# Optimization experiments

Measured on AMD Instinct MI355X. Metric: run time of the kernel, lower is better.

Reference implementation:

```python
import jax, jax.numpy as jnp
import numpy as np

N_NODES = 50000
N_EDGES = 1600000
IN_CH = 128
HID = 128  # 2 * out_channels
NUM_GRAPHS = 64


def gcn_conv(x, row, col, ew, W, b, num_nodes):
    # PyG GCNConv: add self-loops (weight 1), symmetric degree norm, x @ W,
    # gather at source row, scale by norm, scatter-add at target col, add bias.
    loop = jnp.arange(num_nodes)
    r = jnp.concatenate([row, loop])
    c = jnp.concatenate([col, loop])
    w = jnp.concatenate([ew, jnp.ones((num_nodes,), ew.dtype)])
    deg = jax.ops.segment_sum(w, c, num_segments=num_nodes)
    dis = jnp.where(deg > 0, jax.lax.rsqrt(jnp.where(deg > 0, deg, 1.0)), 0.0)
    norm = dis[r] * w * dis[c]  # [E+N]
    xw = x @ W  # [N, HID]
    msg = xw[r] * norm[:, None]  # [E+N, HID] gather + scale
    out = jax.ops.segment_sum(msg, c, num_segments=num_nodes)
    return out + b


def setup_inputs() -> dict:
    key = jax.random.key(0)
    ks = jax.random.split(key, 8)
    x = jax.random.normal(ks[0], (N_NODES, IN_CH), dtype=jnp.float32)
    edge_index = jax.random.randint(ks[1], (2, N_EDGES), 0, N_NODES, dtype=jnp.int64)
    edge_weight = jax.random.uniform(ks[2], (N_EDGES,), dtype=jnp.float32)
    batch = jnp.sort(jax.random.randint(ks[3], (N_NODES,), 0, NUM_GRAPHS, dtype=jnp.int64))
    W1 = jax.random.normal(ks[4], (IN_CH, HID), dtype=jnp.float32) * 0.01
    b1 = jnp.zeros((HID,), jnp.float32)
    W2 = jax.random.normal(ks[5], (HID, HID), dtype=jnp.float32) * 0.01
    b2 = jnp.zeros((HID,), jnp.float32)
    return {"x": x, "edge_index": edge_index, "edge_weight": edge_weight,
            "batch": batch, "W1": W1, "b1": b1, "W2": W2, "b2": b2}


def reference(x, edge_index, edge_weight, batch, W1, b1, W2, b2):
    row, col = edge_index[0], edge_index[1]
    h = jax.nn.relu(gcn_conv(x, row, col, edge_weight, W1, b1, N_NODES))
    h = jax.nn.relu(gcn_conv(h, row, col, edge_weight, W2, b2, N_NODES))
    # global_mean_pool over batch segment ids
    sums = jax.ops.segment_sum(h, batch, num_segments=NUM_GRAPHS)
    cnts = jax.ops.segment_sum(jnp.ones((N_NODES,), h.dtype), batch, num_segments=NUM_GRAPHS)
    pooled = sums / jnp.maximum(cnts, 1.0)[:, None]
    return h, pooled
```

## Files before the change

### kernel.cpp

```cpp
#include <hip/hip_runtime.h>


#define CH 128
#define BSH 7
#define NBLK 1024
#define MAXNB 512
#define PCH 32
#define LDW 136

typedef __attribute__((ext_vector_type(8))) short bf16x8;
typedef __attribute__((ext_vector_type(4))) float f32x4;

static __device__ __forceinline__ unsigned short f2bf(float f) {
    unsigned u = __float_as_uint(f);
    unsigned r = (u + 0x7FFF + ((u >> 16) & 1)) >> 16;
    return (unsigned short)r;
}
static __device__ __forceinline__ float bflo(unsigned v) { return __uint_as_float(v << 16); }
static __device__ __forceinline__ float bfhi(unsigned v) { return __uint_as_float(v & 0xFFFF0000u); }

__global__ __launch_bounds__(256) void k_sort1a(const int* __restrict__ col,
                                                int* __restrict__ H, int E, int NB, int chunk) {
    __shared__ int hist[MAXNB];
    int t = threadIdx.x, blk = blockIdx.x;
    for (int i = t; i < NB; i += 256) hist[i] = 0;
    __syncthreads();
    int s = blk * chunk, e1 = min(s + chunk, E);
    for (int e = s + t; e < e1; e += 256) atomicAdd(&hist[col[e] >> BSH], 1);
    __syncthreads();
    for (int i = t; i < NB; i += 256) H[(size_t)i * NBLK + blk] = hist[i];
}

__global__ __launch_bounds__(1024) void k_scan1(int* __restrict__ data,
                                                int* __restrict__ bsum, int n) {
    __shared__ int sd[1024];
    int t = threadIdx.x;
    int i = blockIdx.x * 1024 + t;
    int v = (i < n) ? data[i] : 0;
    sd[t] = v;
    __syncthreads();
    for (int off = 1; off < 1024; off <<= 1) {
        int u = (t >= off) ? sd[t - off] : 0;
        __syncthreads();
        sd[t] += u;
        __syncthreads();
    }
    if (i < n) data[i] = sd[t] - v;
    if (t == 1023) bsum[blockIdx.x] = sd[1023];
}

__global__ __launch_bounds__(1024) void k_scan2(int* bsum, int nb, int* total) {
    __shared__ int sd[1024];
    int t = threadIdx.x;
    int v = (t < nb) ? bsum[t] : 0;
    sd[t] = v;
    __syncthreads();
    for (int off = 1; off < 1024; off <<= 1) {
        int u = (t >= off) ? sd[t - off] : 0;
        __syncthreads();
        sd[t] += u;
        __syncthreads();
    }
    if (t < nb) bsum[t] = sd[t] - v;
    if (t == 1023) *total = sd[1023];
}

__global__ __launch_bounds__(256) void k_sort1b(const int* __restrict__ row,
                                                const int* __restrict__ col,
                                                const float* __restrict__ ew,
                                                const int* __restrict__ Hs,
                                                const int* __restrict__ bsum,
                                                int2* __restrict__ pairs2,
                                                int E, int NB, int chunk) {
    __shared__ int cur[MAXNB];
    int t = threadIdx.x, blk = blockIdx.x;
    for (int i = t; i < NB; i += 256) cur[i] = Hs[(size_t)i * NBLK + blk] + bsum[i];
    __syncthreads();
    int s = blk * chunk, e1 = min(s + chunk, E);
    for (int e = s + t; e < e1; e += 256) {
        int c = col[e];
        int pos = atomicAdd(&cur[c >> BSH], 1);
        pairs2[pos] = make_int2(row[e] | ((c & 127) << 17), __float_as_int(ew[e]));
    }
}

__global__ __launch_bounds__(256) void k_sort2(const int* __restrict__ Hs,
                                               const int* __restrict__ bsum,
                                               const int2* __restrict__ pairs2,
                                               int2* __restrict__ pairs,
                                               int* __restrict__ rowptr,
                                               float* __restrict__ dis,
                                               int E, int N, int NB) {
    __shared__ int hist[128];
    __shared__ int pref[128];
    __shared__ float wsum[128];
    int b = blockIdx.x, t = threadIdx.x;
    int n0 = b << BSH;
    int s = Hs[(size_t)b * NBLK] + bsum[b];
    int e1 = (b + 1 < NB) ? Hs[(size_t)(b + 1) * NBLK] + bsum[b + 1] : E;
    if (t < 128) { hist[t] = 0; wsum[t] = 0.f; }
    __syncthreads();
    for (int e = s + t; e < e1; e += 256)
        atomicAdd(&hist[(unsigned)pairs2[e].x >> 17], 1);
    __syncthreads();
    if (t < 128) pref[t] = hist[t];
    __syncthreads();
    for (int off = 1; off < 128; off <<= 1) {
        int v = 0;
        if (t < 128 && t >= off) v = pref[t - off];
        __syncthreads();
        if (t < 128) pref[t] += v;
        __syncthreads();
    }
    if (t < 128) {
        int excl = pref[t] - hist[t];
        int node = n0 + t;
        if (node < N) rowptr[node] = s + excl;
        hist[t] = s + excl;
    }
    if (b == NB - 1 && t == 0) rowptr[N] = E;
    __syncthreads();
    for (int e = s + t; e < e1; e += 256) {
        int2 pr = pairs2[e];
        int li = (unsigned)pr.x >> 17;
        int pos = atomicAdd(&hist[li], 1);
        pairs[pos] = make_int2(pr.x & 0x1FFFF, pr.y);
        atomicAdd(&wsum[li], __int_as_float(pr.y));
    }
    __syncthreads();
    if (t < 128 && n0 + t < N) dis[n0 + t] = rsqrtf(1.0f + wsum[t]);
}

__global__ __launch_bounds__(512) void k_gemm(const float* __restrict__ X,
                                              const float* __restrict__ W,
                                              unsigned short* __restrict__ Y, int N) {
    __shared__ unsigned short Wt[128 * LDW];
    int tid = threadIdx.x;
    for (int i = tid; i < 4096; i += 512) {
        float4 v = ((const float4*)W)[i];
        int k = i >> 5;
        int c = (i & 31) * 4;
        Wt[(c + 0) * LDW + k] = f2bf(v.x);
        Wt[(c + 1) * LDW + k] = f2bf(v.y);
        Wt[(c + 2) * LDW + k] = f2bf(v.z);
        Wt[(c + 3) * LDW + k] = f2bf(v.w);
    }
    __syncthreads();
    int w = tid >> 6, lane = tid & 63;
    int l15 = lane & 15, kg = lane >> 4;
    int r = blockIdx.x * 128 + w * 16 + l15;
    f32x4 acc[8];
#pragma unroll
    for (int ct = 0; ct < 8; ++ct) acc[ct] = (f32x4){0.f, 0.f, 0.f, 0.f};
#pragma unroll
    for (int kb = 0; kb < 128; kb += 32) {
        union { unsigned u[4]; bf16x8 v; } a;
        if (r < N) {
            const float4* xp = (const float4*)(X + (size_t)r * CH + kb + kg * 8);
            float4 x0 = xp[0], x1 = xp[1];
            a.u[0] = ((unsigned)f2bf(x0.y) << 16) | f2bf(x0.x);
            a.u[1] = ((unsigned)f2bf(x0.w) << 16) | f2bf(x0.z);
            a.u[2] = ((unsigned)f2bf(x1.y) << 16) | f2bf(x1.x);
            a.u[3] = ((unsigned)f2bf(x1.w) << 16) | f2bf(x1.z);
        } else {
            a.u[0] = a.u[1] = a.u[2] = a.u[3] = 0;
        }
#pragma unroll
        for (int ct = 0; ct < 8; ++ct) {
            bf16x8 b = *(const bf16x8*)&Wt[(ct * 16 + l15) * LDW + kb + kg * 8];
            acc[ct] = __builtin_amdgcn_mfma_f32_16x16x32_bf16(a.v, b, acc[ct], 0, 0, 0);
        }
    }
    int orow = blockIdx.x * 128 + w * 16 + kg * 4;
#pragma unroll
    for (int ct = 0; ct < 8; ++ct) {
#pragma unroll
        for (int j = 0; j < 4; ++j) {
            int rr = orow + j;
            if (rr < N) Y[(size_t)rr * CH + ct * 16 + l15] = f2bf(acc[ct][j]);
        }
    }
}

__global__ __launch_bounds__(64) void k_agg(const unsigned int* __restrict__ XW,
                                            const float* __restrict__ dis,
                                            const int* __restrict__ rowptr,
                                            const int2* __restrict__ pairs,
                                            const float* __restrict__ bias,
                                            float* __restrict__ OUT, int N) {
    int n = blockIdx.x;
    if (n >= N) return;
    int lane = threadIdx.x;
    float dn = dis[n];
    float sn = dn * dn;
    unsigned a = XW[(size_t)n * 64 + lane];
    float ax = bflo(a) * sn;
    float ay = bfhi(a) * sn;
    int e0 = rowptr[n], e1 = rowptr[n + 1];
    int e = e0;
    for (; e + 8 <= e1; e += 8) {
        int2 p0 = pairs[e],     p1 = pairs[e + 1], p2 = pairs[e + 2], p3 = pairs[e + 3];
        int2 p4 = pairs[e + 4], p5 = pairs[e + 5], p6 = pairs[e + 6], p7 = pairs[e + 7];
        unsigned v0 = XW[(size_t)p0.x * 64 + lane];
        unsigned v1 = XW[(size_t)p1.x * 64 + lane];
        unsigned v2 = XW[(size_t)p2.x * 64 + lane];
        unsigned v3 = XW[(size_t)p3.x * 64 + lane];
        unsigned v4 = XW[(size_t)p4.x * 64 + lane];
        unsigned v5 = XW[(size_t)p5.x * 64 + lane];
        unsigned v6 = XW[(size_t)p6.x * 64 + lane];
        unsigned v7 = XW[(size_t)p7.x * 64 + lane];
        float n0 = dn * __int_as_float(p0.y) * dis[p0.x];
        float n1 = dn * __int_as_float(p1.y) * dis[p1.x];
        float n2 = dn * __int_as_float(p2.y) * dis[p2.x];
        float n3 = dn * __int_as_float(p3.y) * dis[p3.x];
        float n4 = dn * __int_as_float(p4.y) * dis[p4.x];
        float n5 = dn * __int_as_float(p5.y) * dis[p5.x];
        float n6 = dn * __int_as_float(p6.y) * dis[p6.x];
        float n7 = dn * __int_as_float(p7.y) * dis[p7.x];
        ax += n0 * bflo(v0) + n1 * bflo(v1) + n2 * bflo(v2) + n3 * bflo(v3)
            + n4 * bflo(v4) + n5 * bflo(v5) + n6 * bflo(v6) + n7 * bflo(v7);
        ay += n0 * bfhi(v0) + n1 * bfhi(v1) + n2 * bfhi(v2) + n3 * bfhi(v3)
            + n4 * bfhi(v4) + n5 * bfhi(v5) + n6 * bfhi(v6) + n7 * bfhi(v7);
    }
    for (; e < e1; ++e) {
        int2 p = pairs[e];
        unsigned v = XW[(size_t)p.x * 64 + lane];
        float nn = dn * __int_as_float(p.y) * dis[p.x];
        ax += nn * bflo(v);
        ay += nn * bfhi(v);
    }
    float2 b = ((const float2*)bias)[lane];
    ax = fmaxf(ax + b.x, 0.f);
    ay = fmaxf(ay + b.y, 0.f);
    ((float2*)OUT)[(size_t)n * 64 + lane] = make_float2(ax, ay);
}

__device__ __forceinline__ int lowerb(const int* a, int n, int v) {
    int lo = 0, hi = n;
    while (lo < hi) {
        int m = (lo + hi) >> 1;
        if (a[m] < v) lo = m + 1; else hi = m;
    }
    return lo;
}

__global__ __launch_bounds__(128) void k_pool1(const float* __restrict__ H,
                                               const int* __restrict__ batch,
                                               float* __restrict__ partial, int N) {
    __shared__ int ss[2];
    int g = blockIdx.x / PCH;
    int k = blockIdx.x % PCH;
    if (threadIdx.x == 0) {
        ss[0] = lowerb(batch, N, g);
        ss[1] = lowerb(batch, N, g + 1);
    }
    __syncthreads();
    int s = ss[0], len = ss[1] - ss[0];
    int cs = s + (int)(((long long)len * k) / PCH);
    int ce = s + (int)(((long long)len * (k + 1)) / PCH);
    int ch = threadIdx.x;
    float a0 = 0.f, a1 = 0.f;
    int n = cs;
    for (; n + 2 <= ce; n += 2) {
        a0 += H[(size_t)(n + 0) * CH + ch];
        a1 += H[(size_t)(n + 1) * CH + ch];
    }
    for (; n < ce; ++n) a0 += H[(size_t)n * CH + ch];
    partial[(size_t)blockIdx.x * CH + ch] = a0 + a1;
}

__global__ __launch_bounds__(128) void k_pool2(const float* __restrict__ partial,
                                               const int* __restrict__ batch,
                                               float* __restrict__ P, int N) {
    __shared__ int ss[2];
    int g = blockIdx.x;
    if (threadIdx.x == 0) {
        ss[0] = lowerb(batch, N, g);
        ss[1] = lowerb(batch, N, g + 1);
    }
    __syncthreads();
    int ch = threadIdx.x;
    float a = 0.f;
#pragma unroll
    for (int k = 0; k < PCH; ++k) a += partial[(size_t)(g * PCH + k) * CH + ch];
    float c = (float)(ss[1] - ss[0]);
    P[(size_t)g * CH + ch] = a / fmaxf(c, 1.f);
}

extern "C" void kernel_launch(void* const* d_in, const int* in_sizes, int n_in,
                              void* d_out, int out_size, void* d_ws, size_t ws_size,
                              hipStream_t stream) {
    const float* x     = (const float*)d_in[0];
    const int*   ei    = (const int*)d_in[1];
    const float* ew    = (const float*)d_in[2];
    const int*   batch = (const int*)d_in[3];
    const float* W1    = (const float*)d_in[4];
    const float* b1    = (const float*)d_in[5];
    const float* W2    = (const float*)d_in[6];
    const float* b2    = (const float*)d_in[7];

    int N = in_sizes[0] / CH;
    int E = in_sizes[1] / 2;
    const int* row = ei;
    const int* col = ei + E;

    float* out    = (float*)d_out;
    float* h      = out;
    float* pooled = out + (size_t)N * CH;

    int NB    = (N + 127) >> BSH;
    int chunk = (E + NBLK - 1) / NBLK;
    int n2    = NB * NBLK;

    char* wsb = (char*)d_ws;
    size_t oN  = ((size_t)N * 4 + 255) & ~(size_t)255;
    size_t oN1 = ((size_t)(N + 1) * 4 + 255) & ~(size_t)255;
    size_t oH  = ((size_t)(n2 + 1) * 4 + 255) & ~(size_t)255;
    size_t oB  = 4096;
    size_t oE2 = ((size_t)E * 8 + 255) & ~(size_t)255;
    float* dis    = (float*)wsb;
    int*   rowptr = (int*)(wsb + oN);
    int*   H      = (int*)(wsb + oN + oN1);
    int*   bsum   = (int*)(wsb + oN + oN1 + oH);
    int2*  pairs  = (int2*)(wsb + oN + oN1 + oH + oB);
    unsigned short* xw = (unsigned short*)(wsb + oN + oN1 + oH + oB + oE2);
    int2*  pairs2 = (int2*)xw;
    float* partial = (float*)H;

    int sb2 = (n2 + 1023) / 1024;

    k_sort1a<<<NBLK, 256, 0, stream>>>(col, H, E, NB, chunk);
    k_scan1<<<sb2, 1024, 0, stream>>>(H, bsum, n2);
    k_scan2<<<1, 1024, 0, stream>>>(bsum, sb2, H + n2);
    k_sort1b<<<NBLK, 256, 0, stream>>>(row, col, ew, H, bsum, pairs2, E, NB, chunk);
    k_sort2<<<NB, 256, 0, stream>>>(H, bsum, pairs2, pairs, rowptr, dis, E, N, NB);

    int gb = (N + 127) / 128;
    k_gemm<<<gb, 512, 0, stream>>>(x, W1, xw, N);
    k_agg<<<N, 64, 0, stream>>>((const unsigned int*)xw, dis, rowptr, pairs, b1, h, N);
    k_gemm<<<gb, 512, 0, stream>>>(h, W2, xw, N);
    k_agg<<<N, 64, 0, stream>>>((const unsigned int*)xw, dis, rowptr, pairs, b2, h, N);
    k_pool1<<<64 * PCH, 128, 0, stream>>>(h, batch, partial, N);
    k_pool2<<<64, 128, 0, stream>>>(partial, batch, pooled, N);
}
```

Measured before the change: 225.0 us.

## Pack edge source and precomputed fp16 norm into one 32-bit word

Edge records shrink from an 8-byte (src, weight) pair to a single 32-bit word: a 17-bit source index plus a 15-bit fp16 value with the sign bit dropped. A new k_norm pass precomputes the full symmetric norm dis[dst]*w*dis[src] into that word once. Both aggregation layers then skip the per-edge dis[src] gather and read half the edge bytes. The cost is an extra kernel launch and fp16 precision on the norms, which relies on weights being non-negative and on node ids fitting in 17 bits.

Result: no change. 223.7 us (-0.5%).

```diff
diff --git a/kernel.cpp b/kernel.cpp
--- a/kernel.cpp
+++ b/kernel.cpp
@@ -1,4 +1,5 @@
 #include <hip/hip_runtime.h>
+#include <hip/hip_fp16.h>
 
 
 #define CH 128
@@ -18,6 +19,14 @@
 }
 static __device__ __forceinline__ float bflo(unsigned v) { return __uint_as_float(v << 16); }
 static __device__ __forceinline__ float bfhi(unsigned v) { return __uint_as_float(v & 0xFFFF0000u); }
+static __device__ __forceinline__ float f16u(unsigned bits15) {
+    __half_raw hr; hr.x = (unsigned short)(bits15 & 0x7FFF);
+    return __half2float(*reinterpret_cast<__half*>(&hr));
+}
+static __device__ __forceinline__ unsigned u16f(float f) {
+    __half hh = __float2half(f);
+    return (unsigned)(*reinterpret_cast<unsigned short*>(&hh)) & 0x7FFF;
+}
 
 __global__ __launch_bounds__(256) void k_sort1a(const int* __restrict__ col,
                                                 int* __restrict__ H, int E, int NB, int chunk) {
@@ -87,7 +96,7 @@
 __global__ __launch_bounds__(256) void k_sort2(const int* __restrict__ Hs,
                                                const int* __restrict__ bsum,
                                                const int2* __restrict__ pairs2,
-                                               int2* __restrict__ pairs,
+                                               unsigned* __restrict__ epk,
                                                int* __restrict__ rowptr,
                                                float* __restrict__ dis,
                                                int E, int N, int NB) {
@@ -123,12 +132,28 @@
     for (int e = s + t; e < e1; e += 256) {
         int2 pr = pairs2[e];
         int li = (unsigned)pr.x >> 17;
+        float w = __int_as_float(pr.y);
         int pos = atomicAdd(&hist[li], 1);
-        pairs[pos] = make_int2(pr.x & 0x1FFFF, pr.y);
-        atomicAdd(&wsum[li], __int_as_float(pr.y));
+        epk[pos] = (unsigned)(pr.x & 0x1FFFF) | (u16f(w) << 17);
+        atomicAdd(&wsum[li], w);
     }
     __syncthreads();
     if (t < 128 && n0 + t < N) dis[n0 + t] = rsqrtf(1.0f + wsum[t]);
+}
+
+__global__ __launch_bounds__(64) void k_norm(const int* __restrict__ rowptr,
+                                             unsigned* __restrict__ epk,
+                                             const float* __restrict__ dis, int N) {
+    int n = blockIdx.x;
+    int lane = threadIdx.x;
+    float dn = dis[n];
+    int e0 = rowptr[n], e1 = rowptr[n + 1];
+    for (int e = e0 + lane; e < e1; e += 64) {
+        unsigned v = epk[e];
+        unsigned src = v & 0x1FFFF;
+        float nn = dn * f16u(v >> 17) * dis[src];
+        epk[e] = src | (u16f(nn) << 17);
+    }
 }
 
 __global__ __launch_bounds__(512) void k_gemm(const float* __restrict__ X,
@@ -185,7 +210,7 @@
 __global__ __launch_bounds__(64) void k_agg(const unsigned int* __restrict__ XW,
                                             const float* __restrict__ dis,
                                             const int* __restrict__ rowptr,
-                                            const int2* __restrict__ pairs,
+                                            const unsigned* __restrict__ epk,
                                             const float* __restrict__ bias,
                                             float* __restrict__ OUT, int N) {
     int n = blockIdx.x;
@@ -199,33 +224,29 @@
     int e0 = rowptr[n], e1 = rowptr[n + 1];
     int e = e0;
     for (; e + 8 <= e1; e += 8) {
-        int2 p0 = pairs[e],     p1 = pairs[e + 1], p2 = pairs[e + 2], p3 = pairs[e + 3];
-        int2 p4 = pairs[e + 4], p5 = pairs[e + 5], p6 = pairs[e + 6], p7 = pairs[e + 7];
-        unsigned v0 = XW[(size_t)p0.x * 64 + lane];
-        unsigned v1 = XW[(size_t)p1.x * 64 + lane];
-        unsigned v2 = XW[(size_t)p2.x * 64 + lane];
-        unsigned v3 = XW[(size_t)p3.x * 64 + lane];
-        unsigned v4 = XW[(size_t)p4.x * 64 + lane];
-        unsigned v5 = XW[(size_t)p5.x * 64 + lane];
-        unsigned v6 = XW[(size_t)p6.x * 64 + lane];
-        unsigned v7 = XW[(size_t)p7.x * 64 + lane];
-        float n0 = dn * __int_as_float(p0.y) * dis[p0.x];
-        float n1 = dn * __int_as_float(p1.y) * dis[p1.x];
-        float n2 = dn * __int_as_float(p2.y) * dis[p2.x];
-        float n3 = dn * __int_as_float(p3.y) * dis[p3.x];
-        float n4 = dn * __int_as_float(p4.y) * dis[p4.x];
-        float n5 = dn * __int_as_float(p5.y) * dis[p5.x];
-        float n6 = dn * __int_as_float(p6.y) * dis[p6.x];
-        float n7 = dn * __int_as_float(p7.y) * dis[p7.x];
+        unsigned p0 = epk[e],     p1 = epk[e + 1], p2 = epk[e + 2], p3 = epk[e + 3];
+        unsigned p4 = epk[e + 4], p5 = epk[e + 5], p6 = epk[e + 6], p7 = epk[e + 7];
+        unsigned v0 = XW[(size_t)(p0 & 0x1FFFF) * 64 + lane];
+        unsigned v1 = XW[(size_t)(p1 & 0x1FFFF) * 64 + lane];
+        unsigned v2 = XW[(size_t)(p2 & 0x1FFFF) * 64 + lane];
+        unsigned v3 = XW[(size_t)(p3 & 0x1FFFF) * 64 + lane];
+        unsigned v4 = XW[(size_t)(p4 & 0x1FFFF) * 64 + lane];
+        unsigned v5 = XW[(size_t)(p5 & 0x1FFFF) * 64 + lane];
+        unsigned v6 = XW[(size_t)(p6 & 0x1FFFF) * 64 + lane];
+        unsigned v7 = XW[(size_t)(p7 & 0x1FFFF) * 64 + lane];
+        float n0 = f16u(p0 >> 17), n1 = f16u(p1 >> 17);
+        float n2 = f16u(p2 >> 17), n3 = f16u(p3 >> 17);
+        float n4 = f16u(p4 >> 17), n5 = f16u(p5 >> 17);
+        float n6 = f16u(p6 >> 17), n7 = f16u(p7 >> 17);
         ax += n0 * bflo(v0) + n1 * bflo(v1) + n2 * bflo(v2) + n3 * bflo(v3)
             + n4 * bflo(v4) + n5 * bflo(v5) + n6 * bflo(v6) + n7 * bflo(v7);
         ay += n0 * bfhi(v0) + n1 * bfhi(v1) + n2 * bfhi(v2) + n3 * bfhi(v3)
             + n4 * bfhi(v4) + n5 * bfhi(v5) + n6 * bfhi(v6) + n7 * bfhi(v7);
     }
     for (; e < e1; ++e) {
-        int2 p = pairs[e];
-        unsigned v = XW[(size_t)p.x * 64 + lane];
-        float nn = dn * __int_as_float(p.y) * dis[p.x];
+        unsigned p = epk[e];
+        unsigned v = XW[(size_t)(p & 0x1FFFF) * 64 + lane];
+        float nn = f16u(p >> 17);
         ax += nn * bflo(v);
         ay += nn * bfhi(v);
     }
@@ -317,13 +338,13 @@
     size_t oN1 = ((size_t)(N + 1) * 4 + 255) & ~(size_t)255;
     size_t oH  = ((size_t)(n2 + 1) * 4 + 255) & ~(size_t)255;
     size_t oB  = 4096;
-    size_t oE2 = ((size_t)E * 8 + 255) & ~(size_t)255;
+    size_t oE1 = ((size_t)E * 4 + 255) & ~(size_t)255;
     float* dis    = (float*)wsb;
     int*   rowptr = (int*)(wsb + oN);
     int*   H      = (int*)(wsb + oN + oN1);
     int*   bsum   = (int*)(wsb + oN + oN1 + oH);
-    int2*  pairs  = (int2*)(wsb + oN + oN1 + oH + oB);
-    unsigned short* xw = (unsigned short*)(wsb + oN + oN1 + oH + oB + oE2);
+    unsigned* epk = (unsigned*)(wsb + oN + oN1 + oH + oB);
+    unsigned short* xw = (unsigned short*)(wsb + oN + oN1 + oH + oB + oE1);
     int2*  pairs2 = (int2*)xw;
     float* partial = (float*)H;
 
@@ -333,13 +354,14 @@
     k_scan1<<<sb2, 1024, 0, stream>>>(H, bsum, n2);
     k_scan2<<<1, 1024, 0, stream>>>(bsum, sb2, H + n2);
     k_sort1b<<<NBLK, 256, 0, stream>>>(row, col, ew, H, bsum, pairs2, E, NB, chunk);
-    k_sort2<<<NB, 256, 0, stream>>>(H, bsum, pairs2, pairs, rowptr, dis, E, N, NB);
+    k_sort2<<<NB, 256, 0, stream>>>(H, bsum, pairs2, epk, rowptr, dis, E, N, NB);
+    k_norm<<<N, 64, 0, stream>>>(rowptr, epk, dis, N);
 
     int gb = (N + 127) / 128;
     k_gemm<<<gb, 512, 0, stream>>>(x, W1, xw, N);
-    k_agg<<<N, 64, 0, stream>>>((const unsigned int*)xw, dis, rowptr, pairs, b1, h, N);
+    k_agg<<<N, 64, 0, stream>>>((const unsigned int*)xw, dis, rowptr, epk, b1, h, N);
     k_gemm<<<gb, 512, 0, stream>>>(h, W2, xw, N);
-    k_agg<<<N, 64, 0, stream>>>((const unsigned int*)xw, dis, rowptr, pairs, b2, h, N);
+    k_agg<<<N, 64, 0, stream>>>((const unsigned int*)xw, dis, rowptr, epk, b2, h, N);
     k_pool1<<<64 * PCH, 128, 0, stream>>>(h, batch, partial, N);
     k_pool2<<<64, 128, 0, stream>>>(partial, batch, pooled, N);
 }
```
